# Optimization experiments

Measured on AMD Instinct MI355X. Metric: run time of the kernel, lower is better.

Reference implementation:

```python
import jax, jax.numpy as jnp
import numpy as np

EMB = 768
HEADS = 12
HD = EMB // HEADS
DFF = 4 * EMB
EPS = 1e-5


def layernorm(x, g, b):
    mu = jnp.mean(x, axis=-1, keepdims=True)
    var = jnp.mean(jnp.square(x - mu), axis=-1, keepdims=True)
    return (x - mu) * jax.lax.rsqrt(var + EPS) * g + b


def setup_inputs() -> dict:
    key = jax.random.key(0)
    ks = jax.random.split(key, 12)
    B, L = 16, 1024
    std = 0.02
    return {
        "x": jax.random.normal(ks[0], (B, L, EMB), jnp.float32),
        "ln1_g": jnp.ones((EMB,), jnp.float32),
        "ln1_b": jnp.zeros((EMB,), jnp.float32),
        "Wq": jax.random.normal(ks[1], (EMB, EMB), jnp.float32) * std,
        "bq": jnp.zeros((EMB,), jnp.float32),
        "Wk": jax.random.normal(ks[2], (EMB, EMB), jnp.float32) * std,
        "bk": jnp.zeros((EMB,), jnp.float32),
        "Wv": jax.random.normal(ks[3], (EMB, EMB), jnp.float32) * std,
        "bv": jnp.zeros((EMB,), jnp.float32),
        "Wo": jax.random.normal(ks[4], (EMB, EMB), jnp.float32) * std,
        "bo": jnp.zeros((EMB,), jnp.float32),
        "ln2_g": jnp.ones((EMB,), jnp.float32),
        "ln2_b": jnp.zeros((EMB,), jnp.float32),
        "W1": jax.random.normal(ks[5], (EMB, DFF), jnp.float32) * std,
        "b1": jnp.zeros((DFF,), jnp.float32),
        "W2": jax.random.normal(ks[6], (DFF, EMB), jnp.float32) * std,
        "b2": jnp.zeros((EMB,), jnp.float32),
    }


def reference(x, ln1_g, ln1_b, Wq, bq, Wk, bk, Wv, bv, Wo, bo,
              ln2_g, ln2_b, W1, b1, W2, b2):
    B, L, D = x.shape
    # --- attention (pre-LN) ---
    h = layernorm(x, ln1_g, ln1_b)
    q = (h @ Wq + bq).reshape(B, L, HEADS, HD)
    k = (h @ Wk + bk).reshape(B, L, HEADS, HD)
    v = (h @ Wv + bv).reshape(B, L, HEADS, HD)
    scores = jnp.einsum("blhd,bmhd->bhlm", q, k) / np.sqrt(HD).astype(np.float32)
    attn = jax.nn.softmax(scores, axis=-1)
    ctx = jnp.einsum("bhlm,bmhd->blhd", attn, v).reshape(B, L, D)
    x = x + ctx @ Wo + bo
    # --- MLP (pre-LN), dropout is identity in eval ---
    h = layernorm(x, ln2_g, ln2_b)
    h = jax.nn.gelu(h @ W1 + b1, approximate=False)  # torch nn.GELU default = exact erf
    x = x + h @ W2 + b2
    return x
```

## Files before the change

### kernel.cpp

```cpp
#include <hip/hip_runtime.h>
#include <hip/hip_bf16.h>
#include <math.h>

#define EMB 768
#define DFF 3072
#define HEADS 12
#define HD 64
#define LSEQ 1024
#define BATCH 16
#define BL (BATCH * LSEQ)
#define QKVD 2304
#define QSCALE 0.1803368801111204f

typedef __attribute__((ext_vector_type(8))) short short8;
typedef __attribute__((ext_vector_type(4))) float floatx4;
typedef unsigned short u16;

__device__ __forceinline__ u16 f2bf(float f) {
  union { float f; unsigned u; } c; c.f = f;
  unsigned u = c.u;
  u += 0x7fffu + ((u >> 16) & 1u);
  return (u16)(u >> 16);
}
__device__ __forceinline__ u16 f2bf_trunc(float f) {
  union { float f; unsigned u; } c; c.f = f;
  return (u16)(c.u >> 16);
}
__device__ __forceinline__ float fast_exp2(float x) {
#if __has_builtin(__builtin_amdgcn_exp2f)
  return __builtin_amdgcn_exp2f(x);
#else
  return exp2f(x);
#endif
}
__device__ __forceinline__ float fast_rcp(float x) {
#if __has_builtin(__builtin_amdgcn_rcpf)
  return __builtin_amdgcn_rcpf(x);
#else
  return 1.0f / x;
#endif
}
__device__ __forceinline__ float gelu_fast(float x) {
  float x2 = x * x;
  float u = x * fmaf(0.10294540f, x2, 2.30211423f);
  u = fminf(fmaxf(u, -30.f), 30.f);
  float t = fast_exp2(u);
  return x * t * fast_rcp(t + 1.0f);
}
__device__ __forceinline__ void async16(const u16* g, u16* l) {
  __builtin_amdgcn_global_load_lds(
      (const __attribute__((address_space(1))) unsigned int*)g,
      (__attribute__((address_space(3))) unsigned int*)l, 16, 0, 0);
}
__device__ __forceinline__ short8 load16(const u16* p) {
  return *reinterpret_cast<const short8*>(p);
}

__global__ __launch_bounds__(256) void ln_kernel(const float* __restrict__ x,
                                                 const float* __restrict__ g,
                                                 const float* __restrict__ b,
                                                 u16* __restrict__ out) {
  int row = blockIdx.x * 4 + (threadIdx.x >> 6);
  int lane = threadIdx.x & 63;
  const float* xr = x + (size_t)row * EMB;
  float v[12];
#pragma unroll
  for (int i = 0; i < 3; i++) {
    float4 t = *reinterpret_cast<const float4*>(xr + i * 256 + lane * 4);
    v[i*4+0] = t.x; v[i*4+1] = t.y; v[i*4+2] = t.z; v[i*4+3] = t.w;
  }
  float s = 0.f, ss = 0.f;
#pragma unroll
  for (int i = 0; i < 12; i++) { s += v[i]; ss += v[i] * v[i]; }
#pragma unroll
  for (int off = 1; off < 64; off <<= 1) {
    s  += __shfl_xor(s, off);
    ss += __shfl_xor(ss, off);
  }
  float mu  = s * (1.f / 768.f);
  float var = ss * (1.f / 768.f) - mu * mu;
  float rs  = rsqrtf(var + 1e-5f);
  u16* orow = out + (size_t)row * EMB;
#pragma unroll
  for (int i = 0; i < 3; i++) {
    int col = i * 256 + lane * 4;
    ushort4 o;
    o.x = f2bf((v[i*4+0] - mu) * rs * g[col+0] + b[col+0]);
    o.y = f2bf((v[i*4+1] - mu) * rs * g[col+1] + b[col+1]);
    o.z = f2bf((v[i*4+2] - mu) * rs * g[col+2] + b[col+2]);
    o.w = f2bf((v[i*4+3] - mu) * rs * g[col+3] + b[col+3]);
    *reinterpret_cast<ushort4*>(orow + col) = o;
  }
}

__global__ void prep_kernel(const float* __restrict__ Wq, const float* __restrict__ Wk,
                            const float* __restrict__ Wv, const float* __restrict__ Wo,
                            const float* __restrict__ W1, const float* __restrict__ W2,
                            u16* __restrict__ wqkv, u16* __restrict__ wot,
                            u16* __restrict__ w1t, u16* __restrict__ w2t,
                            const float* __restrict__ bq, const float* __restrict__ bk,
                            const float* __restrict__ bv, float* __restrict__ obias) {
  __shared__ float t[32][33];
  int id = blockIdx.x;
  int tx = threadIdx.x, ty = threadIdx.y;
  if (id >= 6912) {
    int i = (id - 6912) * 256 + ty * 32 + tx;
    if (i < QKVD)
      obias[i] = i < EMB ? bq[i] : (i < 2*EMB ? bk[i - EMB] : bv[i - 2*EMB]);
    return;
  }
  const float* in; u16* out; int K, N, bx, by;
  if (id < 2304) {
    int seg = id / 576, rem = id % 576;
    bx = rem % 24; by = rem / 24; K = EMB; N = EMB;
    in = seg == 0 ? Wq : seg == 1 ? Wk : seg == 2 ? Wv : Wo;
    out = seg == 3 ? wot : wqkv + (size_t)seg * EMB * EMB;
  } else if (id < 4608) {
    int rem = id - 2304; bx = rem % 96; by = rem / 96;
    in = W1; out = w1t; K = EMB; N = DFF;
  } else {
    int rem = id - 4608; bx = rem % 24; by = rem / 24;
    in = W2; out = w2t; K = DFF; N = EMB;
  }
  int x0 = bx * 32, y0 = by * 32;
#pragma unroll
  for (int i = 0; i < 4; i++)
    t[ty + i*8][tx] = in[(size_t)(y0 + ty + i*8) * N + x0 + tx];
  __syncthreads();
#pragma unroll
  for (int i = 0; i < 4; i++)
    out[(size_t)(x0 + ty + i*8) * K + y0 + tx] = f2bf(t[tx][ty + i*8]);
}

__global__ void vtrans_kernel(const u16* __restrict__ qkv, u16* __restrict__ vt) {
  __shared__ u16 t[32][33];
  int l0 = blockIdx.x * 32;
  int d0 = blockIdx.y * 32;
  int bh = blockIdx.z;
  int b = bh / HEADS, h = bh % HEADS;
  int tx = threadIdx.x, ty = threadIdx.y;
#pragma unroll
  for (int i = 0; i < 4; i++)
    t[ty + i*8][tx] = qkv[(size_t)(b * LSEQ + l0 + ty + i*8) * QKVD + 2*EMB + h * HD + d0 + tx];
  __syncthreads();
#pragma unroll
  for (int i = 0; i < 4; i++)
    vt[(size_t)(bh * HD + d0 + ty + i*8) * LSEQ + l0 + tx] = t[tx][ty + i*8];
}

#define BK 64
__global__ __launch_bounds__(256) void gemm_kernel(
    const u16* __restrict__ A, const u16* __restrict__ Bt,
    const float* __restrict__ bias, const float* __restrict__ res,
    u16* __restrict__ outb, float* __restrict__ outf,
    int M, int N, int K, int mode, float scale, int scale_n) {
  __shared__ u16 As[128 * BK];
  __shared__ u16 Bs[128 * BK];
  int tid = threadIdx.x;
  int lane = tid & 63, wave = tid >> 6;
  int wm = wave & 1, wn = wave >> 1;
  int l16 = lane & 15, lhi = lane >> 4;
  int m0 = blockIdx.x * 128, n0 = blockIdx.y * 128;

  floatx4 acc[4][4];
#pragma unroll
  for (int i = 0; i < 4; i++)
#pragma unroll
    for (int j = 0; j < 4; j++) acc[i][j] = {0.f, 0.f, 0.f, 0.f};

  int rr = lane >> 3;
  int cs = ((lane & 7) ^ rr) * 8;
  const u16* aptr = A + (size_t)(m0 + wave * 32 + rr) * K + cs;
  const u16* bptr = Bt + (size_t)(n0 + wave * 32 + rr) * K + cs;
  u16* asl = As + (wave * 32) * BK;
  u16* bsl = Bs + (wave * 32) * BK;

  int l7 = l16 & 7;
  int oa0 = (wm * 64 + l16) * BK + ((lhi ^ l7) * 8);
  int ob0 = (wn * 64 + l16) * BK + ((lhi ^ l7) * 8);
  int oa1 = oa0 ^ 32;
  int ob1 = ob0 ^ 32;

  for (int k0 = 0; k0 < K; k0 += BK) {
    __syncthreads();
#pragma unroll
    for (int i = 0; i < 4; i++) {
      async16(aptr + (size_t)(i * 8) * K + k0, asl + i * 8 * BK);
      async16(bptr + (size_t)(i * 8) * K + k0, bsl + i * 8 * BK);
    }
    __syncthreads();
#pragma unroll
    for (int kk = 0; kk < 2; kk++) {
      int oA = kk ? oa1 : oa0;
      int oB = kk ? ob1 : ob0;
      short8 af[4], bfr[4];
#pragma unroll
      for (int mt = 0; mt < 4; mt++)
        af[mt] = *reinterpret_cast<const short8*>(&As[oA + mt * 16 * BK]);
#pragma unroll
      for (int nt = 0; nt < 4; nt++)
        bfr[nt] = *reinterpret_cast<const short8*>(&Bs[oB + nt * 16 * BK]);
#pragma unroll
      for (int mt = 0; mt < 4; mt++)
#pragma unroll
        for (int nt = 0; nt < 4; nt++)
          acc[mt][nt] = __builtin_amdgcn_mfma_f32_16x16x32_bf16(bfr[nt], af[mt],
                                                                acc[mt][nt], 0, 0, 0);
    }
  }

#pragma unroll
  for (int mt = 0; mt < 4; mt++) {
    int m = m0 + wm*64 + mt*16 + l16;
#pragma unroll
    for (int nt = 0; nt < 4; nt++) {
      int nbase = n0 + wn*64 + nt*16 + lhi*4;
      float4 bv = *reinterpret_cast<const float4*>(&bias[nbase]);
      float v0 = acc[mt][nt][0] + bv.x, v1 = acc[mt][nt][1] + bv.y;
      float v2 = acc[mt][nt][2] + bv.z, v3 = acc[mt][nt][3] + bv.w;
      if (mode == 1) {
        float4 r = *reinterpret_cast<const float4*>(&res[(size_t)m * N + nbase]);
        float4 o; o.x = v0 + r.x; o.y = v1 + r.y; o.z = v2 + r.z; o.w = v3 + r.w;
        *reinterpret_cast<float4*>(&outf[(size_t)m * N + nbase]) = o;
      } else {
        if (mode == 2) {
          v0 = gelu_fast(v0); v1 = gelu_fast(v1);
          v2 = gelu_fast(v2); v3 = gelu_fast(v3);
        } else {
          float sc = (nbase < scale_n) ? scale : 1.0f;
          v0 *= sc; v1 *= sc; v2 *= sc; v3 *= sc;
        }
        ushort4 o;
        o.x = f2bf(v0); o.y = f2bf(v1); o.z = f2bf(v2); o.w = f2bf(v3);
        *reinterpret_cast<ushort4*>(&outb[(size_t)m * N + nbase]) = o;
      }
    }
  }
}

#define PSTRIDE 76
__global__ __launch_bounds__(256) void flash_kernel(
    const u16* __restrict__ qkv, const u16* __restrict__ vt,
    u16* __restrict__ ctx) {
  __shared__ u16 Kb[2][64 * 64];
  __shared__ u16 Vb[2][64 * 64];
  __shared__ u16 Ps[4][2][16][PSTRIDE];
  int tid = threadIdx.x;
  int lane = tid & 63, w = tid >> 6;
  int l16 = lane & 15, lhi = lane >> 4;

  int i = blockIdx.x;
  int bh = (i & 7) | ((i >> 5) << 3);
  int qb = (i >> 3) & 3;
  int b = bh / HEADS, h = bh % HEADS;
  int q0 = qb * 256 + w * 64;

  const u16* qbase = qkv + (size_t)(b * LSEQ) * QKVD + h * HD;
  const u16* kbase = qbase + EMB;
  const u16* vbase = vt + (size_t)(bh * HD) * LSEQ;

  int rr = lane >> 3;
  int c8 = (lane & 7) ^ rr;
  const u16* ksrc = kbase + (size_t)(w * 16 + rr) * QKVD + c8 * 8;
  const u16* vsrc = vbase + (size_t)(w * 16 + rr) * LSEQ + c8 * 8;

#pragma unroll
  for (int j = 0; j < 2; j++) {
    async16(ksrc + (size_t)(j * 8) * QKVD, &Kb[0][(w * 16 + j * 8) * 64]);
    async16(vsrc + (size_t)(j * 8) * LSEQ, &Vb[0][(w * 16 + j * 8) * 64]);
  }

  short8 qf[4][2];
#pragma unroll
  for (int st = 0; st < 4; st++)
#pragma unroll
    for (int kk = 0; kk < 2; kk++)
      qf[st][kk] = load16(qbase + (size_t)(q0 + st*16 + l16) * QKVD + kk*32 + lhi*8);

  floatx4 o[4][4];
#pragma unroll
  for (int st = 0; st < 4; st++)
#pragma unroll
    for (int mt = 0; mt < 4; mt++) o[st][mt] = {0.f, 0.f, 0.f, 0.f};
  float l_i[4] = {0.f, 0.f, 0.f, 0.f};

  __syncthreads();

  int cur = 0;
  for (int kt = 0; kt < LSEQ; kt += 64) {
    if (kt + 64 < LSEQ) {
      const u16* kn = ksrc + (size_t)(kt + 64) * QKVD;
      const u16* vn = vsrc + (kt + 64);
#pragma unroll
      for (int j = 0; j < 2; j++) {
        async16(kn + (size_t)(j * 8) * QKVD, &Kb[cur ^ 1][(w * 16 + j * 8) * 64]);
        async16(vn + (size_t)(j * 8) * LSEQ, &Vb[cur ^ 1][(w * 16 + j * 8) * 64]);
      }
    }

    short8 kf[4][2], vf[4][2];
#pragma unroll
    for (int mt = 0; mt < 4; mt++) {
      int krow = mt * 16 + l16;
#pragma unroll
      for (int kk = 0; kk < 2; kk++) {
        int slot = ((kk * 4 + lhi) ^ (krow & 7)) * 8;
        kf[mt][kk] = load16(&Kb[cur][krow * 64 + slot]);
        vf[mt][kk] = load16(&Vb[cur][krow * 64 + slot]);
      }
    }

#pragma unroll
    for (int st = 0; st < 4; st++) {
      u16* pbuf = &Ps[w][st & 1][0][0];
      floatx4 s[4];
#pragma unroll
      for (int mt = 0; mt < 4; mt++) s[mt] = {0.f, 0.f, 0.f, 0.f};
#pragma unroll
      for (int mt = 0; mt < 4; mt++)
#pragma unroll
        for (int kk = 0; kk < 2; kk++)
          s[mt] = __builtin_amdgcn_mfma_f32_16x16x32_bf16(kf[mt][kk], qf[st][kk],
                                                          s[mt], 0, 0, 0);
      float ls = 0.f;
#pragma unroll
      for (int mt = 0; mt < 4; mt++) {
        ushort4 pw;
        float p0 = fast_exp2(s[mt][0]), p1 = fast_exp2(s[mt][1]);
        float p2 = fast_exp2(s[mt][2]), p3 = fast_exp2(s[mt][3]);
        ls += (p0 + p1) + (p2 + p3);
        pw.x = f2bf_trunc(p0); pw.y = f2bf_trunc(p1);
        pw.z = f2bf_trunc(p2); pw.w = f2bf_trunc(p3);
        *reinterpret_cast<ushort4*>(&pbuf[l16 * PSTRIDE + mt*16 + lhi*4]) = pw;
      }
      l_i[st] += ls;
      short8 pf0 = load16(&pbuf[l16 * PSTRIDE + 0*32 + lhi*8]);
      short8 pf1 = load16(&pbuf[l16 * PSTRIDE + 1*32 + lhi*8]);
#pragma unroll
      for (int mt = 0; mt < 4; mt++) {
        o[st][mt] = __builtin_amdgcn_mfma_f32_16x16x32_bf16(vf[mt][0], pf0,
                                                            o[st][mt], 0, 0, 0);
        o[st][mt] = __builtin_amdgcn_mfma_f32_16x16x32_bf16(vf[mt][1], pf1,
                                                            o[st][mt], 0, 0, 0);
      }
    }

    __syncthreads();
    cur ^= 1;
  }

#pragma unroll
  for (int st = 0; st < 4; st++) {
    l_i[st] += __shfl_xor(l_i[st], 16);
    l_i[st] += __shfl_xor(l_i[st], 32);
  }

#pragma unroll
  for (int st = 0; st < 4; st++) {
    float inv = fast_rcp(l_i[st]);
    size_t rowbase = (size_t)(b * LSEQ + q0 + st*16 + l16) * EMB + h * HD;
#pragma unroll
    for (int mt = 0; mt < 4; mt++) {
      ushort4 ow;
      ow.x = f2bf(o[st][mt][0] * inv); ow.y = f2bf(o[st][mt][1] * inv);
      ow.z = f2bf(o[st][mt][2] * inv); ow.w = f2bf(o[st][mt][3] * inv);
      *reinterpret_cast<ushort4*>(&ctx[rowbase + mt*16 + lhi*4]) = ow;
    }
  }
}

extern "C" void kernel_launch(void* const* d_in, const int* in_sizes, int n_in,
                              void* d_out, int out_size, void* d_ws, size_t ws_size,
                              hipStream_t stream) {
  const float* x    = (const float*)d_in[0];
  const float* ln1g = (const float*)d_in[1];
  const float* ln1b = (const float*)d_in[2];
  const float* Wq   = (const float*)d_in[3];
  const float* bq   = (const float*)d_in[4];
  const float* Wk   = (const float*)d_in[5];
  const float* bk   = (const float*)d_in[6];
  const float* Wv   = (const float*)d_in[7];
  const float* bv   = (const float*)d_in[8];
  const float* Wo   = (const float*)d_in[9];
  const float* bo   = (const float*)d_in[10];
  const float* ln2g = (const float*)d_in[11];
  const float* ln2b = (const float*)d_in[12];
  const float* W1   = (const float*)d_in[13];
  const float* b1   = (const float*)d_in[14];
  const float* W2   = (const float*)d_in[15];
  const float* b2   = (const float*)d_in[16];

  char* ws = (char*)d_ws;
  u16* qkv_bf = (u16*)(ws);
  u16* vt_bf  = (u16*)(ws + (size_t)75497472);
  u16* h_bf   = (u16*)(ws + (size_t)100663296);
  float* x2   = (float*)(ws + (size_t)125829120);
  u16* m_bf   = (u16*)(ws);
  char* wp = ws + (size_t)176160768;
  u16* wqkv = (u16*)(wp);
  u16* wot  = (u16*)(wp + (size_t)3538944);
  u16* w1t  = (u16*)(wp + (size_t)3538944 + 1179648);
  u16* w2t  = (u16*)(wp + (size_t)3538944 + 1179648 + 4718592);
  float* qkvbias = (float*)(wp + (size_t)3538944 + 1179648 + 2*4718592);

  dim3 b256(256), tb(32, 8);

  prep_kernel<<<dim3(6921), tb, 0, stream>>>(Wq, Wk, Wv, Wo, W1, W2,
      wqkv, wot, w1t, w2t, bq, bk, bv, qkvbias);

  ln_kernel<<<dim3(BL/4), b256, 0, stream>>>(x, ln1g, ln1b, h_bf);

  gemm_kernel<<<dim3(128, 18), b256, 0, stream>>>(h_bf, wqkv, qkvbias, nullptr,
      qkv_bf, nullptr, BL, QKVD, EMB, 0, QSCALE, EMB);

  vtrans_kernel<<<dim3(32, 2, BATCH*HEADS), tb, 0, stream>>>(qkv_bf, vt_bf);

  flash_kernel<<<dim3(768), b256, 0, stream>>>(qkv_bf, vt_bf, h_bf);

  gemm_kernel<<<dim3(128, 6), b256, 0, stream>>>(h_bf, wot, bo, x, nullptr, x2,
      BL, EMB, EMB, 1, 1.0f, 0);

  ln_kernel<<<dim3(BL/4), b256, 0, stream>>>(x2, ln2g, ln2b, h_bf);

  gemm_kernel<<<dim3(128, 24), b256, 0, stream>>>(h_bf, w1t, b1, nullptr, m_bf,
      nullptr, BL, DFF, EMB, 2, 1.0f, 0);

  gemm_kernel<<<dim3(128, 6), b256, 0, stream>>>(m_bf, w2t, b2, x2, nullptr,
      (float*)d_out, BL, EMB, DFF, 1, 1.0f, 0);
}
```

Baseline: 566.1 us.

## Replace 128x128 GEMM with double-buffered 256x256 tile kernel and block swizzle

Swaps the single-buffered 128x128 bf16 MFMA GEMM for a 512-thread kernel that computes a 256x256 output tile per block. Loads of the next K-slice are split into four staged async copies and interleaved with four MFMA phases, using explicit vmcnt waits, barriers and raised wave priority. Block IDs are also swizzled across M/N tiles for cache locality. The larger tile raises data reuse per block but uses 128KB of shared memory and cuts the grid to 192 blocks for the N=768 GEMMs, which may leave CUs idle.

```diff
diff --git a/kernel.cpp b/kernel.cpp
--- a/kernel.cpp
+++ b/kernel.cpp
@@ -148,76 +148,114 @@
     vt[(size_t)(bh * HD + d0 + ty + i*8) * LSEQ + l0 + tx] = t[tx][ty + i*8];
 }
 
-#define BK 64
-__global__ __launch_bounds__(256) void gemm_kernel(
+#define GPHASE(CUR, MH, NH, STAGE, WAITS)                                      \
+  {                                                                            \
+    short8 af[4][2], bfr[2][2];                                                \
+    _Pragma("unroll")                                                          \
+    for (int mt = 0; mt < 4; mt++) {                                           \
+      int ra = wm * 128 + (MH) * 64 + mt * 16 + l16;                           \
+      int ba = ra * 64 + ((lhi ^ l7) * 8);                                     \
+      af[mt][0] = load16(&As[CUR][ba]);                                        \
+      af[mt][1] = load16(&As[CUR][ba ^ 32]);                                   \
+    }                                                                          \
+    _Pragma("unroll")                                                          \
+    for (int nt = 0; nt < 2; nt++) {                                           \
+      int rb = wn * 64 + (NH) * 32 + nt * 16 + l16;                            \
+      int bb = rb * 64 + ((lhi ^ l7) * 8);                                     \
+      bfr[nt][0] = load16(&Bs[CUR][bb]);                                       \
+      bfr[nt][1] = load16(&Bs[CUR][bb ^ 32]);                                  \
+    }                                                                          \
+    STAGE;                                                                     \
+    __builtin_amdgcn_s_barrier();                                              \
+    __builtin_amdgcn_sched_barrier(0);                                         \
+    __builtin_amdgcn_s_setprio(1);                                             \
+    _Pragma("unroll")                                                          \
+    for (int mt = 0; mt < 4; mt++)                                             \
+      _Pragma("unroll")                                                        \
+      for (int nt = 0; nt < 2; nt++) {                                         \
+        acc[(MH)*4+mt][(NH)*2+nt] = __builtin_amdgcn_mfma_f32_16x16x32_bf16(   \
+            bfr[nt][0], af[mt][0], acc[(MH)*4+mt][(NH)*2+nt], 0, 0, 0);        \
+        acc[(MH)*4+mt][(NH)*2+nt] = __builtin_amdgcn_mfma_f32_16x16x32_bf16(   \
+            bfr[nt][1], af[mt][1], acc[(MH)*4+mt][(NH)*2+nt], 0, 0, 0);        \
+      }                                                                        \
+    __builtin_amdgcn_s_setprio(0);                                             \
+    asm volatile(WAITS ::: "memory");                                          \
+    __builtin_amdgcn_s_barrier();                                              \
+    __builtin_amdgcn_sched_barrier(0);                                         \
+  }
+
+__global__ __launch_bounds__(512, 2) void gemm256_kernel(
     const u16* __restrict__ A, const u16* __restrict__ Bt,
     const float* __restrict__ bias, const float* __restrict__ res,
     u16* __restrict__ outb, float* __restrict__ outf,
     int M, int N, int K, int mode, float scale, int scale_n) {
-  __shared__ u16 As[128 * BK];
-  __shared__ u16 Bs[128 * BK];
+  __shared__ u16 As[2][256 * 64];
+  __shared__ u16 Bs[2][256 * 64];
   int tid = threadIdx.x;
   int lane = tid & 63, wave = tid >> 6;
-  int wm = wave & 1, wn = wave >> 1;
-  int l16 = lane & 15, lhi = lane >> 4;
-  int m0 = blockIdx.x * 128, n0 = blockIdx.y * 128;
-
-  floatx4 acc[4][4];
-#pragma unroll
-  for (int i = 0; i < 4; i++)
+  int wm = wave >> 2, wn = wave & 3;
+  int l16 = lane & 15, lhi = lane >> 4, l7 = l16 & 7;
+
+  int nwg = gridDim.x * gridDim.y;
+  int bid = blockIdx.y * gridDim.x + blockIdx.x;
+  int q = nwg >> 3;
+  int swz = (bid & 7) * q + (bid >> 3);
+  int m0 = (swz & 63) * 256;
+  int n0 = (swz >> 6) * 256;
+
+  floatx4 acc[8][4];
+#pragma unroll
+  for (int i = 0; i < 8; i++)
 #pragma unroll
     for (int j = 0; j < 4; j++) acc[i][j] = {0.f, 0.f, 0.f, 0.f};
 
   int rr = lane >> 3;
   int cs = ((lane & 7) ^ rr) * 8;
-  const u16* aptr = A + (size_t)(m0 + wave * 32 + rr) * K + cs;
-  const u16* bptr = Bt + (size_t)(n0 + wave * 32 + rr) * K + cs;
-  u16* asl = As + (wave * 32) * BK;
-  u16* bsl = Bs + (wave * 32) * BK;
-
-  int l7 = l16 & 7;
-  int oa0 = (wm * 64 + l16) * BK + ((lhi ^ l7) * 8);
-  int ob0 = (wn * 64 + l16) * BK + ((lhi ^ l7) * 8);
-  int oa1 = oa0 ^ 32;
-  int ob1 = ob0 ^ 32;
-
-  for (int k0 = 0; k0 < K; k0 += BK) {
-    __syncthreads();
-#pragma unroll
-    for (int i = 0; i < 4; i++) {
-      async16(aptr + (size_t)(i * 8) * K + k0, asl + i * 8 * BK);
-      async16(bptr + (size_t)(i * 8) * K + k0, bsl + i * 8 * BK);
-    }
-    __syncthreads();
-#pragma unroll
-    for (int kk = 0; kk < 2; kk++) {
-      int oA = kk ? oa1 : oa0;
-      int oB = kk ? ob1 : ob0;
-      short8 af[4], bfr[4];
-#pragma unroll
-      for (int mt = 0; mt < 4; mt++)
-        af[mt] = *reinterpret_cast<const short8*>(&As[oA + mt * 16 * BK]);
-#pragma unroll
-      for (int nt = 0; nt < 4; nt++)
-        bfr[nt] = *reinterpret_cast<const short8*>(&Bs[oB + nt * 16 * BK]);
-#pragma unroll
-      for (int mt = 0; mt < 4; mt++)
-#pragma unroll
-        for (int nt = 0; nt < 4; nt++)
-          acc[mt][nt] = __builtin_amdgcn_mfma_f32_16x16x32_bf16(bfr[nt], af[mt],
-                                                                acc[mt][nt], 0, 0, 0);
-    }
-  }
-
-#pragma unroll
-  for (int mt = 0; mt < 4; mt++) {
-    int m = m0 + wm*64 + mt*16 + l16;
-#pragma unroll
-    for (int nt = 0; nt < 4; nt++) {
-      int nbase = n0 + wn*64 + nt*16 + lhi*4;
+  const u16* aptr = A + (size_t)(m0 + wave * 8 + rr) * K + cs;
+  const u16* bptr = Bt + (size_t)(n0 + (wave >> 2) * 64 + (wave & 3) * 8 + rr) * K + cs;
+
+  auto stageA = [&](int nb, int h, int k0) {
+#pragma unroll
+    for (int j = 0; j < 2; j++)
+      async16(aptr + (size_t)(j * 128 + h * 64) * K + k0,
+              &As[nb][(j * 128 + h * 64 + wave * 8) * 64]);
+  };
+  auto stageB = [&](int nb, int nh, int k0) {
+#pragma unroll
+    for (int j = 0; j < 2; j++)
+      async16(bptr + (size_t)(j * 128 + nh * 32) * K + k0,
+              &Bs[nb][(j * 128 + (wave >> 2) * 64 + nh * 32 + (wave & 3) * 8) * 64]);
+  };
+
+  stageA(0, 0, 0); stageB(0, 0, 0); stageA(0, 1, 0); stageB(0, 1, 0);
+  asm volatile("s_waitcnt vmcnt(0)" ::: "memory");
+  __builtin_amdgcn_s_barrier();
+  __builtin_amdgcn_sched_barrier(0);
+
+  int NT = K >> 6;
+  int cur = 0;
+  for (int t = 0; t < NT - 1; t++) {
+    int kn = (t + 1) << 6;
+    GPHASE(cur, 0, 0, stageA(cur ^ 1, 0, kn), "s_waitcnt vmcnt(4)");
+    GPHASE(cur, 1, 0, stageB(cur ^ 1, 0, kn), "s_waitcnt vmcnt(4)");
+    GPHASE(cur, 0, 1, stageA(cur ^ 1, 1, kn), "s_waitcnt vmcnt(4)");
+    GPHASE(cur, 1, 1, stageB(cur ^ 1, 1, kn), "s_waitcnt vmcnt(4)");
+    cur ^= 1;
+  }
+  GPHASE(cur, 0, 0, , "s_waitcnt vmcnt(0)");
+  GPHASE(cur, 1, 0, , "s_waitcnt vmcnt(0)");
+  GPHASE(cur, 0, 1, , "s_waitcnt vmcnt(0)");
+  GPHASE(cur, 1, 1, , "s_waitcnt vmcnt(0)");
+
+#pragma unroll
+  for (int mi = 0; mi < 8; mi++) {
+    int m = m0 + wm * 128 + mi * 16 + l16;
+#pragma unroll
+    for (int ni = 0; ni < 4; ni++) {
+      int nbase = n0 + wn * 64 + ni * 16 + lhi * 4;
       float4 bv = *reinterpret_cast<const float4*>(&bias[nbase]);
-      float v0 = acc[mt][nt][0] + bv.x, v1 = acc[mt][nt][1] + bv.y;
-      float v2 = acc[mt][nt][2] + bv.z, v3 = acc[mt][nt][3] + bv.w;
+      float v0 = acc[mi][ni][0] + bv.x, v1 = acc[mi][ni][1] + bv.y;
+      float v2 = acc[mi][ni][2] + bv.z, v3 = acc[mi][ni][3] + bv.w;
       if (mode == 1) {
         float4 r = *reinterpret_cast<const float4*>(&res[(size_t)m * N + nbase]);
         float4 o; o.x = v0 + r.x; o.y = v1 + r.y; o.z = v2 + r.z; o.w = v3 + r.w;
@@ -403,28 +441,28 @@
   u16* w2t  = (u16*)(wp + (size_t)3538944 + 1179648 + 4718592);
   float* qkvbias = (float*)(wp + (size_t)3538944 + 1179648 + 2*4718592);
 
-  dim3 b256(256), tb(32, 8);
+  dim3 b256(256), b512(512), tb(32, 8);
 
   prep_kernel<<<dim3(6921), tb, 0, stream>>>(Wq, Wk, Wv, Wo, W1, W2,
       wqkv, wot, w1t, w2t, bq, bk, bv, qkvbias);
 
   ln_kernel<<<dim3(BL/4), b256, 0, stream>>>(x, ln1g, ln1b, h_bf);
 
-  gemm_kernel<<<dim3(128, 18), b256, 0, stream>>>(h_bf, wqkv, qkvbias, nullptr,
+  gemm256_kernel<<<dim3(64, 9), b512, 0, stream>>>(h_bf, wqkv, qkvbias, nullptr,
       qkv_bf, nullptr, BL, QKVD, EMB, 0, QSCALE, EMB);
 
   vtrans_kernel<<<dim3(32, 2, BATCH*HEADS), tb, 0, stream>>>(qkv_bf, vt_bf);
 
   flash_kernel<<<dim3(768), b256, 0, stream>>>(qkv_bf, vt_bf, h_bf);
 
-  gemm_kernel<<<dim3(128, 6), b256, 0, stream>>>(h_bf, wot, bo, x, nullptr, x2,
+  gemm256_kernel<<<dim3(64, 3), b512, 0, stream>>>(h_bf, wot, bo, x, nullptr, x2,
       BL, EMB, EMB, 1, 1.0f, 0);
 
   ln_kernel<<<dim3(BL/4), b256, 0, stream>>>(x2, ln2g, ln2b, h_bf);
 
-  gemm_kernel<<<dim3(128, 24), b256, 0, stream>>>(h_bf, w1t, b1, nullptr, m_bf,
+  gemm256_kernel<<<dim3(64, 12), b512, 0, stream>>>(h_bf, w1t, b1, nullptr, m_bf,
       nullptr, BL, DFF, EMB, 2, 1.0f, 0);
 
-  gemm_kernel<<<dim3(128, 6), b256, 0, stream>>>(m_bf, w2t, b2, x2, nullptr,
+  gemm256_kernel<<<dim3(64, 3), b512, 0, stream>>>(m_bf, w2t, b2, x2, nullptr,
       (float*)d_out, BL, EMB, DFF, 1, 1.0f, 0);
 }
```

After: 674.5 us. 19.2% more time.

## Add 256x256-tile 8-wave bf16 MFMA GEMM for QKV and MLP projections

Applied to the files above, without the earlier changes.

Adds a 512-thread GEMM kernel that computes 256x256 output tiles with double-buffered 64-wide K slices in LDS. Each k-step is split into four phases, with the next tile's async prefetch issued in the first phase and s_setprio raised around the MFMA bursts. It replaces the 128x128 GEMM for the QKV, W1 and W2 projections to raise operand reuse per LDS load and cut global traffic. The cost is 128KB of LDS per block, so only one block fits per CU. Grids also get coarser: the W2 GEMM now launches just 192 blocks, which may leave CUs idle.

```diff
diff --git a/kernel.cpp b/kernel.cpp
--- a/kernel.cpp
+++ b/kernel.cpp
@@ -238,6 +238,116 @@
   }
 }
 
+__global__ __launch_bounds__(512, 2) void gemm256_kernel(
+    const u16* __restrict__ A, const u16* __restrict__ Bt,
+    const float* __restrict__ bias, const float* __restrict__ res,
+    u16* __restrict__ outb, float* __restrict__ outf,
+    int M, int N, int K, int mode, float scale, int scale_n) {
+  __shared__ u16 As[2][256 * 64];
+  __shared__ u16 Bs[2][256 * 64];
+  int tid = threadIdx.x;
+  int lane = tid & 63, wave = tid >> 6;
+  int wm = wave >> 2, wn = wave & 3;
+  int l16 = lane & 15, lhi = lane >> 4, l7 = l16 & 7;
+  int m0 = blockIdx.x * 256, n0 = blockIdx.y * 256;
+
+  floatx4 acc[8][4];
+#pragma unroll
+  for (int i = 0; i < 8; i++)
+#pragma unroll
+    for (int j = 0; j < 4; j++) acc[i][j] = {0.f, 0.f, 0.f, 0.f};
+
+  int rr = lane >> 3;
+  int cs = ((lane & 7) ^ rr) * 8;
+  const u16* aptr = A + (size_t)(m0 + wave * 8 + rr) * K + cs;
+  const u16* bptr = Bt + (size_t)(n0 + wave * 8 + rr) * K + cs;
+
+  auto stage_all = [&](int nb, int k0) {
+#pragma unroll
+    for (int g = 0; g < 4; g++)
+      async16(aptr + (size_t)(g * 64) * K + k0, &As[nb][(g * 64 + wave * 8) * 64]);
+#pragma unroll
+    for (int g = 0; g < 4; g++)
+      async16(bptr + (size_t)(g * 64) * K + k0, &Bs[nb][(g * 64 + wave * 8) * 64]);
+  };
+
+  stage_all(0, 0);
+  asm volatile("s_waitcnt vmcnt(0)" ::: "memory");
+  __builtin_amdgcn_s_barrier();
+  asm volatile("" ::: "memory");
+
+  int oa = (wm * 128 + l16) * 64 + ((lhi ^ l7) * 8);
+  int ob = (wn * 64 + l16) * 64 + ((lhi ^ l7) * 8);
+  short8 bfr[4];
+
+  int NT = K >> 6;
+  for (int t = 0; t < NT; t++) {
+    int cur = t & 1;
+    const u16* pa = As[cur];
+    const u16* pb = Bs[cur];
+    bool pre = (t + 1 < NT);
+#pragma unroll
+    for (int ph = 0; ph < 4; ph++) {
+      int mh = ph & 1, kk = ph >> 1;
+      short8 af[4];
+#pragma unroll
+      for (int mt4 = 0; mt4 < 4; mt4++) {
+        int o = oa + (mh * 64 + mt4 * 16) * 64;
+        af[mt4] = load16(&pa[kk ? (o ^ 32) : o]);
+      }
+      if (mh == 0) {
+#pragma unroll
+        for (int nt = 0; nt < 4; nt++) {
+          int o = ob + nt * 16 * 64;
+          bfr[nt] = load16(&pb[kk ? (o ^ 32) : o]);
+        }
+      }
+      if (ph == 0 && pre) stage_all(cur ^ 1, (t + 1) << 6);
+      __builtin_amdgcn_s_barrier();
+      asm volatile("" ::: "memory");
+      __builtin_amdgcn_s_setprio(1);
+#pragma unroll
+      for (int mt4 = 0; mt4 < 4; mt4++)
+#pragma unroll
+        for (int nt = 0; nt < 4; nt++)
+          acc[mh * 4 + mt4][nt] = __builtin_amdgcn_mfma_f32_16x16x32_bf16(
+              bfr[nt], af[mt4], acc[mh * 4 + mt4][nt], 0, 0, 0);
+      __builtin_amdgcn_s_setprio(0);
+      if (ph == 3 && pre) asm volatile("s_waitcnt vmcnt(0)" ::: "memory");
+      __builtin_amdgcn_s_barrier();
+      asm volatile("" ::: "memory");
+    }
+  }
+
+#pragma unroll
+  for (int mi = 0; mi < 8; mi++) {
+    int m = m0 + wm * 128 + mi * 16 + l16;
+#pragma unroll
+    for (int ni = 0; ni < 4; ni++) {
+      int nbase = n0 + wn * 64 + ni * 16 + lhi * 4;
+      float4 bv = *reinterpret_cast<const float4*>(&bias[nbase]);
+      float v0 = acc[mi][ni][0] + bv.x, v1 = acc[mi][ni][1] + bv.y;
+      float v2 = acc[mi][ni][2] + bv.z, v3 = acc[mi][ni][3] + bv.w;
+      if (mode == 1) {
+        float4 r = *reinterpret_cast<const float4*>(&res[(size_t)m * N + nbase]);
+        float4 o; o.x = v0 + r.x; o.y = v1 + r.y; o.z = v2 + r.z; o.w = v3 + r.w;
+        *reinterpret_cast<float4*>(&outf[(size_t)m * N + nbase]) = o;
+      } else {
+        if (mode == 2) {
+          v0 = gelu_fast(v0); v1 = gelu_fast(v1);
+          v2 = gelu_fast(v2); v3 = gelu_fast(v3);
+        } else {
+          float sc = (nbase < scale_n) ? scale : 1.0f;
+          v0 *= sc; v1 *= sc; v2 *= sc; v3 *= sc;
+        }
+        ushort4 o;
+        o.x = f2bf(v0); o.y = f2bf(v1); o.z = f2bf(v2); o.w = f2bf(v3);
+        *reinterpret_cast<ushort4*>(&outb[(size_t)m * N + nbase]) = o;
+      }
+    }
+  }
+}
+
 #define PSTRIDE 76
 __global__ __launch_bounds__(256) void flash_kernel(
     const u16* __restrict__ qkv, const u16* __restrict__ vt,
@@ -403,14 +513,14 @@
   u16* w2t  = (u16*)(wp + (size_t)3538944 + 1179648 + 4718592);
   float* qkvbias = (float*)(wp + (size_t)3538944 + 1179648 + 2*4718592);
 
-  dim3 b256(256), tb(32, 8);
+  dim3 b256(256), b512(512), tb(32, 8);
 
   prep_kernel<<<dim3(6921), tb, 0, stream>>>(Wq, Wk, Wv, Wo, W1, W2,
       wqkv, wot, w1t, w2t, bq, bk, bv, qkvbias);
 
   ln_kernel<<<dim3(BL/4), b256, 0, stream>>>(x, ln1g, ln1b, h_bf);
 
-  gemm_kernel<<<dim3(128, 18), b256, 0, stream>>>(h_bf, wqkv, qkvbias, nullptr,
+  gemm256_kernel<<<dim3(64, 9), b512, 0, stream>>>(h_bf, wqkv, qkvbias, nullptr,
       qkv_bf, nullptr, BL, QKVD, EMB, 0, QSCALE, EMB);
 
   vtrans_kernel<<<dim3(32, 2, BATCH*HEADS), tb, 0, stream>>>(qkv_bf, vt_bf);
@@ -422,9 +532,9 @@
 
   ln_kernel<<<dim3(BL/4), b256, 0, stream>>>(x2, ln2g, ln2b, h_bf);
 
-  gemm_kernel<<<dim3(128, 24), b256, 0, stream>>>(h_bf, w1t, b1, nullptr, m_bf,
+  gemm256_kernel<<<dim3(64, 12), b512, 0, stream>>>(h_bf, w1t, b1, nullptr, m_bf,
       nullptr, BL, DFF, EMB, 2, 1.0f, 0);
 
-  gemm_kernel<<<dim3(128, 6), b256, 0, stream>>>(m_bf, w2t, b2, x2, nullptr,
+  gemm256_kernel<<<dim3(64, 3), b512, 0, stream>>>(m_bf, w2t, b2, x2, nullptr,
       (float*)d_out, BL, EMB, DFF, 1, 1.0f, 0);
 }
```

Measured after the change: 603.7 us. 1.07x slower.
